# Optimization experiments

Measured on AMD Instinct MI355X. Metric: run time of the kernel, lower is better.

The kernel has to match this reference:

```python
import jax, jax.numpy as jnp
import numpy as np

B, S, D, H = 32, 512, 512, 8  # note: source requires S == D due to swapped shape tuple in multi_head_attention
DK = D // H  # 64
FF = 200     # hard-coded FFN width in source
LN_EPS = 1e-5


def setup_inputs() -> dict:
    key = jax.random.key(0)
    ks = jax.random.split(key, 20)
    s = 0.02
    return {
        "x": jax.random.normal(ks[0], (B, S, D), dtype=jnp.float32),
        # per-head projections, stacked: torch Linear weight shape is [out, in] = [DK, D]
        "Wq": jax.random.normal(ks[1], (H, DK, D), dtype=jnp.float32) * s,
        "bq": jax.random.normal(ks[2], (H, DK), dtype=jnp.float32) * s,
        "Wk": jax.random.normal(ks[3], (H, DK, D), dtype=jnp.float32) * s,
        "bk": jax.random.normal(ks[4], (H, DK), dtype=jnp.float32) * s,
        "Wv": jax.random.normal(ks[5], (H, DK, D), dtype=jnp.float32) * s,
        "bv": jax.random.normal(ks[6], (H, DK), dtype=jnp.float32) * s,
        "Wo": jax.random.normal(ks[7], (D, D), dtype=jnp.float32) * s,
        "bo": jax.random.normal(ks[8], (D,), dtype=jnp.float32) * s,
        "W1": jax.random.normal(ks[9], (FF, D), dtype=jnp.float32) * s,
        "b1": jax.random.normal(ks[10], (FF,), dtype=jnp.float32) * s,
        "W2": jax.random.normal(ks[11], (FF, FF), dtype=jnp.float32) * s,
        "b2": jax.random.normal(ks[12], (FF,), dtype=jnp.float32) * s,
        "W3": jax.random.normal(ks[13], (D, FF), dtype=jnp.float32) * s,
        "b3": jax.random.normal(ks[14], (D,), dtype=jnp.float32) * s,
        # single SHARED LayerNorm over last two dims (S, D)
        "gamma": jnp.ones((S, D), dtype=jnp.float32),
        "beta": jnp.zeros((S, D), dtype=jnp.float32),
    }


def _layernorm2d(y, gamma, beta):
    # torch LayerNorm(normalized_shape=(S, D)): normalize over last two axes, biased variance
    m = jnp.mean(y, axis=(-2, -1), keepdims=True)
    v = jnp.mean(jnp.square(y - m), axis=(-2, -1), keepdims=True)
    return (y - m) * jax.lax.rsqrt(v + LN_EPS) * gamma + beta


def reference(x, Wq, bq, Wk, bk, Wv, bv, Wo, bo, W1, b1, W2, b2, W3, b3, gamma, beta):
    # --- multi-head attention (vectorized over the original per-head Python loop) ---
    q = jnp.einsum('bsd,hkd->bhsk', x, Wq) + bq[None, :, None, :]
    k = jnp.einsum('bsd,hkd->bhsk', x, Wk) + bk[None, :, None, :]
    v = jnp.einsum('bsd,hkd->bhsk', x, Wv) + bv[None, :, None, :]
    scores = jnp.einsum('bhsk,bhtk->bhst', q, k) / jnp.sqrt(jnp.float32(DK))
    attn = jax.nn.softmax(scores, axis=-1)
    heads = jnp.einsum('bhst,bhtk->bhsk', attn, v)          # [B,H,S,DK]
    concat = heads.transpose(0, 2, 1, 3).reshape(B, S, D)    # concat heads along feature dim
    y = jnp.einsum('bsd,ed->bse', concat, Wo) + bo + x       # output proj + residual
    # --- post-attention LayerNorm (shared params) ---
    y = _layernorm2d(y, gamma, beta)
    # --- feed-forward: D -> 200 -> 200 -> D, residual, LayerNorm (same shared LN) ---
    f = jax.nn.relu(jnp.einsum('bsd,fd->bsf', y, W1) + b1)
    f = jax.nn.relu(jnp.einsum('bsf,gf->bsg', f, W2) + b2)
    f = jnp.einsum('bsf,df->bsd', f, W3) + b3
    y = _layernorm2d(f + y, gamma, beta)
    # --- final LayerNorm (same shared LN again) ---
    return _layernorm2d(y, gamma, beta)
```

## Files before the change

kernel.cpp:

```cpp
#include <hip/hip_runtime.h>
#include <hip/hip_bf16.h>
#include <stdint.h>

#define B_  32
#define S_  512
#define D_  512
#define H_  8
#define DK_ 64
#define FF_ 200
#define FFP 256
#define M_  (B_*S_)
#define MSD ((size_t)B_*S_*D_)
#define NQKV 1536

typedef __hip_bfloat16 bf16;
typedef __attribute__((ext_vector_type(8))) short short8;
typedef __attribute__((ext_vector_type(4))) float f32x4;
typedef __attribute__((ext_vector_type(4))) unsigned short us4;

__device__ inline float b2f(bf16 v) { return __bfloat162float(v); }
__device__ inline bf16  f2b(float v){ return __float2bfloat16(v); }
__device__ inline unsigned short f2bu(float v) {
  union { bf16 h; unsigned short u; } cv; cv.h = __float2bfloat16(v); return cv.u;
}
__device__ inline float bu2f(unsigned short u) {
  union { unsigned short u; bf16 h; } cv; cv.u = u; return b2f(cv.h);
}
__device__ __forceinline__ void async16(const bf16* g, bf16* l) {
  __builtin_amdgcn_global_load_lds((const __attribute__((address_space(1))) void*)g,
                                   (__attribute__((address_space(3))) void*)l, 16, 0, 0);
}

__global__ void detect_kernel(const unsigned short* __restrict__ xu, int* __restrict__ flag,
                              float* __restrict__ stats) {
  __shared__ int mx[256];
  const int tid = threadIdx.x;
  if (tid < 192) stats[tid] = 0.f;
  int m = 0;
  for (int i = tid * 2; i < 8192; i += 512) {
    int e = (xu[i] >> 7) & 0xFF;
    m = m > e ? m : e;
  }
  mx[tid] = m;
  __syncthreads();
  for (int st = 128; st; st >>= 1) {
    if (tid < st) mx[tid] = mx[tid] > mx[tid + st] ? mx[tid] : mx[tid + st];
    __syncthreads();
  }
  if (tid == 0) *flag = (mx[0] >= 0xC0) ? 1 : 0;
}

__global__ __launch_bounds__(256) void cvt_x8(const void* __restrict__ in, bf16* __restrict__ out,
                                              const int* __restrict__ flag) {
  const bool f32in = (*flag != 0);
  size_t i = ((size_t)blockIdx.x * 256 + threadIdx.x) * 8;
  const size_t stride = (size_t)gridDim.x * 256 * 8;
  for (; i < MSD; i += stride) {
    if (f32in) {
      const float4 a = ((const float4*)in)[i/4];
      const float4 b = ((const float4*)in)[i/4 + 1];
      uint4 o; unsigned short* po = (unsigned short*)&o;
      po[0]=f2bu(a.x); po[1]=f2bu(a.y); po[2]=f2bu(a.z); po[3]=f2bu(a.w);
      po[4]=f2bu(b.x); po[5]=f2bu(b.y); po[6]=f2bu(b.z); po[7]=f2bu(b.w);
      *(uint4*)((unsigned short*)out + i) = o;
    } else {
      *(uint4*)((unsigned short*)out + i) = *(const uint4*)((const unsigned short*)in + i);
    }
  }
}

struct Seg { const void* src; void* dst; int srcRows, srcK, dstK, total; };
struct Segs { Seg s[16]; unsigned int isbf; };

__global__ __launch_bounds__(256) void cvt_all(Segs sg, const int* __restrict__ flag) {
  const bool f32in = (*flag != 0);
  const int seg = blockIdx.x & 15;
  const Seg sd = sg.s[seg];
  const int stride = (gridDim.x >> 4) * 256;
  const bool nopad = (sd.srcK == sd.dstK);
  for (int i = (blockIdx.x >> 4) * 256 + threadIdx.x; i < sd.total; i += stride) {
    int sidx; bool valid;
    if (nopad) { sidx = i; valid = (i < sd.srcRows * sd.srcK); }
    else {
      int r = i / sd.dstK, c = i - r * sd.dstK;
      valid = (r < sd.srcRows) && (c < sd.srcK);
      sidx = r * sd.srcK + c;
    }
    float v = 0.f;
    if (valid) v = f32in ? ((const float*)sd.src)[sidx] : b2f(((const bf16*)sd.src)[sidx]);
    if (sg.isbf & (1u << seg)) ((unsigned short*)sd.dst)[i] = f2bu(v);
    else                       ((float*)sd.dst)[i] = v;
  }
}

template<int MODE, int STATS>
__global__ __launch_bounds__(256) void gemm_mfma(
    const bf16* __restrict__ A, const bf16* __restrict__ W, const float* __restrict__ bias,
    const bf16* __restrict__ R, bf16* __restrict__ C, int M, int N, int K,
    float* __restrict__ stats)
{
  __shared__ __align__(16) char smem[49152];
  bf16*  As  = (bf16*)smem;
  bf16*  Bs  = (bf16*)(smem + 24576);
  float* Lf  = (float*)smem;
  float* red = (float*)(smem + 16896);

  const int tid  = threadIdx.x;
  const int bm   = blockIdx.x * 128;
  const int bn   = blockIdx.y * 128;
  const int w    = tid >> 6;
  const int lane = tid & 63;
  const int qd   = lane >> 4;
  const int ln   = lane & 15;
  const int wr   = (w >> 1) * 64;
  const int wc   = (w & 1) * 64;

  const int r0 = lane >> 2;
  const int ch = (lane & 3) * 8;
  const bf16* Ag0 = A + (size_t)(bm + w*16 + r0) * K + ch;
  const bf16* Ag1 = Ag0 + (size_t)64 * K;
  const bf16* Bg0 = W + (size_t)(bn + w*16 + r0) * K + ch;
  const bf16* Bg1 = Bg0 + (size_t)64 * K;
  const int lo = w*512 + lane*8;

  f32x4 acc[4][4] = {};
  const int nt = K >> 5;

  async16(Ag0, As + lo);
  async16(Ag1, As + lo + 2048);
  async16(Bg0, Bs + lo);
  async16(Bg1, Bs + lo + 2048);
  async16(Ag0 + 32, As + 4096 + lo);
  async16(Ag1 + 32, As + 4096 + lo + 2048);
  async16(Bg0 + 32, Bs + 4096 + lo);
  async16(Bg1 + 32, Bs + 4096 + lo + 2048);

  int pcur = 0;
  for (int t = 0; t < nt; t++) {
    if (t + 1 < nt) {
      asm volatile("s_waitcnt vmcnt(4)" ::: "memory");
    } else {
      asm volatile("s_waitcnt vmcnt(0)" ::: "memory");
    }
    __builtin_amdgcn_s_barrier();

    const int cur = pcur << 12;
    short8 af[4], bfr[4];
#pragma unroll
    for (int i = 0; i < 4; i++) af[i]  = *(const short8*)(As + cur + (wr + i*16 + ln)*32 + qd*8);
#pragma unroll
    for (int j = 0; j < 4; j++) bfr[j] = *(const short8*)(Bs + cur + (wc + j*16 + ln)*32 + qd*8);

    if (t + 2 < nt) {
      int pst = pcur - 1; if (pst < 0) pst = 2;
      const int nxt = pst << 12;
      const int k0  = (t + 2) << 5;
      async16(Ag0 + k0, As + nxt + lo);
      async16(Ag1 + k0, As + nxt + lo + 2048);
      async16(Bg0 + k0, Bs + nxt + lo);
      async16(Bg1 + k0, Bs + nxt + lo + 2048);
    }

#pragma unroll
    for (int i = 0; i < 4; i++)
#pragma unroll
      for (int j = 0; j < 4; j++)
        acc[i][j] = __builtin_amdgcn_mfma_f32_16x16x32_bf16(af[i], bfr[j], acc[i][j], 0, 0, 0);

    pcur = pcur + 1 == 3 ? 0 : pcur + 1;
  }
  __syncthreads();

  float s_acc = 0.f, ss_acc = 0.f;
  const int lrbase = (w >> 1)*16 + qd*4;
#pragma unroll
  for (int i = 0; i < 4; i++) {
#pragma unroll
    for (int j = 0; j < 4; j++) {
      const int col = wc + j*16 + ln;
#pragma unroll
      for (int rg = 0; rg < 4; rg++)
        Lf[(lrbase + rg)*132 + col] = acc[i][j][rg];
    }
    __syncthreads();
#pragma unroll
    for (int pz = 0; pz < 2; pz++) {
      const int q   = tid + pz*256;
      const int r   = q >> 4;
      const int nof = (q & 15)*8;
      const int m   = bm + (r >> 4)*64 + i*16 + (r & 15);
      const int n   = bn + nof;
      f32x4 v0 = *(const f32x4*)(Lf + r*132 + nof);
      f32x4 v1 = *(const f32x4*)(Lf + r*132 + nof + 4);
      f32x4 b0 = *(const f32x4*)(bias + n);
      f32x4 b1 = *(const f32x4*)(bias + n + 4);
      float vals[8];
#pragma unroll
      for (int e = 0; e < 4; e++) { vals[e] = v0[e] + b0[e]; vals[4+e] = v1[e] + b1[e]; }
      if (MODE == 1) {
#pragma unroll
        for (int e = 0; e < 8; e++) vals[e] = fmaxf(vals[e], 0.f);
      }
      if (MODE == 2) {
        const uint4 rv = *(const uint4*)((const unsigned short*)R + (size_t)m * N + n);
        const unsigned short* rp = (const unsigned short*)&rv;
#pragma unroll
        for (int e = 0; e < 8; e++) vals[e] += bu2f(rp[e]);
      }
      if (STATS) {
#pragma unroll
        for (int e = 0; e < 8; e++) { s_acc += vals[e]; ss_acc += vals[e]*vals[e]; }
      }
      uint4 o; unsigned short* op = (unsigned short*)&o;
#pragma unroll
      for (int e = 0; e < 8; e++) op[e] = f2bu(vals[e]);
      *(uint4*)((unsigned short*)C + (size_t)m * N + n) = o;
    }
    __syncthreads();
  }

  if (STATS) {
    red[tid] = s_acc; red[256 + tid] = ss_acc;
    __syncthreads();
    for (int st = 128; st; st >>= 1) {
      if (tid < st) { red[tid] += red[tid + st]; red[256 + tid] += red[256 + tid + st]; }
      __syncthreads();
    }
    if (tid == 0) {
      const int b = bm >> 9;
      atomicAdd(&stats[b*2],     red[0]);
      atomicAdd(&stats[b*2 + 1], red[256]);
    }
  }
}

__global__ __launch_bounds__(1024, 4) void attn_lds(const bf16* __restrict__ qkv,
                                                    bf16* __restrict__ cat)
{
  __shared__ bf16 Ks[2 * 512 * 32];
  __shared__ bf16 Vs[64 * 520];
  __shared__ bf16 pbuf[16][16][40];

  const int tid  = threadIdx.x;
  const int w    = tid >> 6;
  const int lane = tid & 63;
  const int qd   = lane >> 4;
  const int ln   = lane & 15;
  const int bh   = blockIdx.x;
  const int b    = bh >> 3, h = bh & 7;
  const bf16* base = qkv + (size_t)b * 512 * NQKV + h * 64;

  for (int c = tid; c < 4096; c += 1024) {
    int part = c & 3, key = (c >> 2) & 511, ks = c >> 11;
    async16(base + (size_t)key * NQKV + 512 + ks*32 + part*8, Ks + c*8);
  }
  for (int c = tid; c < 4096; c += 1024) {
    int dkg = c >> 9, key = c & 511;
    uint4 vv = *(const uint4*)(base + (size_t)key * NQKV + 1024 + dkg*8);
    const unsigned short* pv = (const unsigned short*)&vv;
#pragma unroll
    for (int j = 0; j < 8; j++)
      *(unsigned short*)&Vs[(dkg*8 + j)*520 + key] = pv[j];
  }
  short8 bq[2][2];
#pragma unroll
  for (int qt = 0; qt < 2; qt++)
#pragma unroll
    for (int ks = 0; ks < 2; ks++)
      bq[qt][ks] = *(const short8*)(base + (size_t)(w*32 + qt*16 + ln) * NQKV + ks*32 + qd*8);

  __syncthreads();

  bf16 (*pb)[40] = pbuf[w];
  f32x4 o[2][4] = {};
  float l[2] = {0.f, 0.f};

  for (int st = 0; st < 16; st++) {
    short8 ak[2][2];
#pragma unroll
    for (int kt = 0; kt < 2; kt++)
#pragma unroll
      for (int ks = 0; ks < 2; ks++)
        ak[kt][ks] = *(const short8*)(Ks + ks*16384 + (st*32 + kt*16 + ln)*32 + qd*8);
    f32x4 s[2][2] = {};
#pragma unroll
    for (int kt = 0; kt < 2; kt++)
#pragma unroll
      for (int qt = 0; qt < 2; qt++) {
        s[kt][qt] = __builtin_amdgcn_mfma_f32_16x16x32_bf16(ak[kt][0], bq[qt][0], s[kt][qt], 0, 0, 0);
        s[kt][qt] = __builtin_amdgcn_mfma_f32_16x16x32_bf16(ak[kt][1], bq[qt][1], s[kt][qt], 0, 0, 0);
      }
    float e[2][2][4];
#pragma unroll
    for (int kt = 0; kt < 2; kt++)
#pragma unroll
      for (int qt = 0; qt < 2; qt++)
#pragma unroll
        for (int rg = 0; rg < 4; rg++) {
          float ev = __expf(s[kt][qt][rg] * 0.125f);
          e[kt][qt][rg] = ev;
          l[qt] += ev;
        }
#pragma unroll
    for (int qt = 0; qt < 2; qt++) {
#pragma unroll
      for (int kt = 0; kt < 2; kt++) {
        uint2 pk;
        pk.x = (unsigned)f2bu(e[kt][qt][0]) | ((unsigned)f2bu(e[kt][qt][1]) << 16);
        pk.y = (unsigned)f2bu(e[kt][qt][2]) | ((unsigned)f2bu(e[kt][qt][3]) << 16);
        *(uint2*)&pb[ln][kt*16 + qd*4] = pk;
      }
      short8 ap = *(const short8*)&pb[ln][qd*8];
#pragma unroll
      for (int nt = 0; nt < 4; nt++) {
        short8 bv = *(const short8*)(Vs + (nt*16 + ln)*520 + st*32 + qd*8);
        o[qt][nt] = __builtin_amdgcn_mfma_f32_16x16x32_bf16(ap, bv, o[qt][nt], 0, 0, 0);
      }
    }
  }

#pragma unroll
  for (int qt = 0; qt < 2; qt++) {
    l[qt] += __shfl_xor(l[qt], 16);
    l[qt] += __shfl_xor(l[qt], 32);
  }
  float inv0 = 1.f / l[0], inv1 = 1.f / l[1];

  const size_t crow0 = (size_t)(b*S_ + w*32) * D_ + h*DK_;
#pragma unroll
  for (int qt = 0; qt < 2; qt++) {
#pragma unroll
    for (int rg = 0; rg < 4; rg++) {
      float ivv = __shfl(qt ? inv1 : inv0, qd*4 + rg);
      int r = qt*16 + qd*4 + rg;
      bf16* cp = cat + crow0 + (size_t)r * D_ + ln;
#pragma unroll
      for (int nt = 0; nt < 4; nt++) cp[nt*16] = f2b(o[qt][nt][rg] * ivv);
    }
  }
}

__global__ __launch_bounds__(256) void ln_b16_b16(const bf16* __restrict__ in,
    const float* __restrict__ stats, const bf16* __restrict__ gamma,
    const bf16* __restrict__ beta, bf16* __restrict__ out)
{
  const int b = blockIdx.x >> 4;
  const float invN = 1.f / (float)(S_*D_);
  const float m    = stats[b*2] * invN;
  const float var  = stats[b*2+1] * invN - m*m;
  const float rstd = rsqrtf(var + 1e-5f);
  size_t v = (size_t)b * 65536 + (blockIdx.x & 15) * 4096 + threadIdx.x;
#pragma unroll 4
  for (int it = 0; it < 16; it++, v += 256) {
    us4 xi = *(const us4*)((const unsigned short*)in + v*4);
    size_t e = (v * 4) & (S_*D_ - 1);
    us4 g4 = *(const us4*)((const unsigned short*)gamma + e);
    us4 b4 = *(const us4*)((const unsigned short*)beta + e);
    us4 o;
    o[0] = f2bu((bu2f(xi[0]) - m) * rstd * bu2f(g4[0]) + bu2f(b4[0]));
    o[1] = f2bu((bu2f(xi[1]) - m) * rstd * bu2f(g4[1]) + bu2f(b4[1]));
    o[2] = f2bu((bu2f(xi[2]) - m) * rstd * bu2f(g4[2]) + bu2f(b4[2]));
    o[3] = f2bu((bu2f(xi[3]) - m) * rstd * bu2f(g4[3]) + bu2f(b4[3]));
    *(us4*)((unsigned short*)out + v*4) = o;
  }
}

__global__ __launch_bounds__(256) void ln_b16_b16_stats(const bf16* __restrict__ in,
    const float* __restrict__ stats, const bf16* __restrict__ gamma,
    const bf16* __restrict__ beta, bf16* __restrict__ out, float* __restrict__ stats3)
{
  __shared__ float red[512];
  const int b = blockIdx.x >> 4;
  const float invN = 1.f / (float)(S_*D_);
  const float m    = stats[b*2] * invN;
  const float var  = stats[b*2+1] * invN - m*m;
  const float rstd = rsqrtf(var + 1e-5f);
  size_t v = (size_t)b * 65536 + (blockIdx.x & 15) * 4096 + threadIdx.x;
  float s_acc = 0.f, ss_acc = 0.f;
#pragma unroll 4
  for (int it = 0; it < 16; it++, v += 256) {
    us4 xi = *(const us4*)((const unsigned short*)in + v*4);
    size_t e = (v * 4) & (S_*D_ - 1);
    us4 g4 = *(const us4*)((const unsigned short*)gamma + e);
    us4 b4 = *(const us4*)((const unsigned short*)beta + e);
    float o0 = (bu2f(xi[0]) - m) * rstd * bu2f(g4[0]) + bu2f(b4[0]);
    float o1 = (bu2f(xi[1]) - m) * rstd * bu2f(g4[1]) + bu2f(b4[1]);
    float o2 = (bu2f(xi[2]) - m) * rstd * bu2f(g4[2]) + bu2f(b4[2]);
    float o3 = (bu2f(xi[3]) - m) * rstd * bu2f(g4[3]) + bu2f(b4[3]);
    us4 o;
    o[0] = f2bu(o0); o[1] = f2bu(o1); o[2] = f2bu(o2); o[3] = f2bu(o3);
    s_acc  += o0 + o1 + o2 + o3;
    ss_acc += o0*o0 + o1*o1 + o2*o2 + o3*o3;
    *(us4*)((unsigned short*)out + v*4) = o;
  }
  const int tid = threadIdx.x;
  red[tid] = s_acc; red[256 + tid] = ss_acc;
  __syncthreads();
  for (int st = 128; st; st >>= 1) {
    if (tid < st) { red[tid] += red[tid + st]; red[256 + tid] += red[256 + tid + st]; }
    __syncthreads();
  }
  if (tid == 0) {
    atomicAdd(&stats3[b*2],     red[0]);
    atomicAdd(&stats3[b*2 + 1], red[256]);
  }
}

__global__ __launch_bounds__(256) void ln_apply_out(const bf16* __restrict__ in,
    const float* __restrict__ stats, const bf16* __restrict__ gamma,
    const bf16* __restrict__ beta, void* __restrict__ out, const int* __restrict__ flag)
{
  const bool f32 = (*flag != 0);
  const int b = blockIdx.x >> 4;
  const float invN = 1.f / (float)(S_*D_);
  const float m    = stats[b*2] * invN;
  const float var  = stats[b*2+1] * invN - m*m;
  const float rstd = rsqrtf(var + 1e-5f);
  size_t v = (size_t)b * 65536 + (blockIdx.x & 15) * 4096 + threadIdx.x;
#pragma unroll 4
  for (int it = 0; it < 16; it++, v += 256) {
    us4 xi = *(const us4*)((const unsigned short*)in + v*4);
    size_t e = (v * 4) & (S_*D_ - 1);
    us4 g4 = *(const us4*)((const unsigned short*)gamma + e);
    us4 b4 = *(const us4*)((const unsigned short*)beta + e);
    float4 o;
    o.x = (bu2f(xi[0]) - m) * rstd * bu2f(g4[0]) + bu2f(b4[0]);
    o.y = (bu2f(xi[1]) - m) * rstd * bu2f(g4[1]) + bu2f(b4[1]);
    o.z = (bu2f(xi[2]) - m) * rstd * bu2f(g4[2]) + bu2f(b4[2]);
    o.w = (bu2f(xi[3]) - m) * rstd * bu2f(g4[3]) + bu2f(b4[3]);
    if (f32) ((float4*)out)[v] = o;
    else {
      us4 ob;
      ob[0] = f2bu(o.x); ob[1] = f2bu(o.y); ob[2] = f2bu(o.z); ob[3] = f2bu(o.w);
      *(us4*)((unsigned short*)out + v*4) = ob;
    }
  }
}

extern "C" void kernel_launch(void* const* d_in, const int* in_sizes, int n_in,
                              void* d_out, int out_size, void* d_ws, size_t ws_size,
                              hipStream_t stream)
{
  char* p = (char*)d_ws;
  auto alloc_b = [&](size_t elems) { void* r = p; p += elems * 2; return (bf16*)r; };
  auto alloc_f = [&](size_t elems) {
    p = (char*)(((uintptr_t)p + 15) & ~(uintptr_t)15); void* r = p; p += elems * 4; return (float*)r;
  };

  bf16* xb   = alloc_b(MSD);
  bf16* qkv  = alloc_b(3 * MSD);
  bf16* catb = alloc_b(MSD);
  bf16* wqkv = alloc_b(3 * 512 * 512);
  bf16* wo   = alloc_b(512 * 512);
  bf16* w1p  = alloc_b((size_t)FFP * 512);
  bf16* w2p  = alloc_b((size_t)FFP * FFP);
  bf16* w3p  = alloc_b((size_t)512 * FFP);
  bf16* gm   = alloc_b((size_t)S_ * D_);
  bf16* bt   = alloc_b((size_t)S_ * D_);
  float* bqkv= alloc_f(3 * 512);
  float* bo  = alloc_f(512);
  float* b1p = alloc_f(FFP);
  float* b2p = alloc_f(FFP);
  float* b3  = alloc_f(512);
  float* stats = alloc_f(192);
  int*   flag  = (int*)alloc_f(16);
  if ((size_t)(p - (char*)d_ws) > ws_size) return;

  bf16* y1b = qkv;
  bf16* f1  = qkv + MSD;
  bf16* f2  = qkv + MSD + (size_t)M_ * FFP;
  bf16* yA  = qkv + 2 * MSD;
  bf16* yB  = catb;
  bf16* y2b = yA;
  float* st1 = stats, *st2 = stats + 64, *st3 = stats + 128;

  detect_kernel<<<1, 256, 0, stream>>>((const unsigned short*)d_in[0], flag, stats);
  cvt_x8<<<2048, 256, 0, stream>>>(d_in[0], xb, flag);

  Segs sg;
  sg.s[0]  = { d_in[1],  wqkv,               512, 512, 512, 512*512 };
  sg.s[1]  = { d_in[3],  wqkv + 512*512,     512, 512, 512, 512*512 };
  sg.s[2]  = { d_in[5],  wqkv + 2*512*512,   512, 512, 512, 512*512 };
  sg.s[3]  = { d_in[7],  wo,                 512, 512, 512, 512*512 };
  sg.s[4]  = { d_in[9],  w1p,                FF_, 512, 512, FFP*512 };
  sg.s[5]  = { d_in[11], w2p,                FF_, FF_, FFP, FFP*FFP };
  sg.s[6]  = { d_in[13], w3p,                512, FF_, FFP, 512*FFP };
  sg.s[7]  = { d_in[2],  bqkv,               1, 512, 512, 512 };
  sg.s[8]  = { d_in[4],  bqkv + 512,         1, 512, 512, 512 };
  sg.s[9]  = { d_in[6],  bqkv + 1024,        1, 512, 512, 512 };
  sg.s[10] = { d_in[8],  bo,                 1, 512, 512, 512 };
  sg.s[11] = { d_in[10], b1p,                1, FF_, FFP, FFP };
  sg.s[12] = { d_in[12], b2p,                1, FF_, FFP, FFP };
  sg.s[13] = { d_in[14], b3,                 1, 512, 512, 512 };
  sg.s[14] = { d_in[15], gm,                 1, S_*D_, S_*D_, S_*D_ };
  sg.s[15] = { d_in[16], bt,                 1, S_*D_, S_*D_, S_*D_ };
  sg.isbf = 0xC07F;
  cvt_all<<<1024, 256, 0, stream>>>(sg, flag);

  dim3 blk(256);

  gemm_mfma<0, 0><<<dim3(M_/128, NQKV/128), blk, 0, stream>>>(
      xb, wqkv, bqkv, nullptr, qkv, M_, NQKV, 512, nullptr);

  attn_lds<<<B_*H_, 1024, 0, stream>>>(qkv, catb);

  gemm_mfma<2, 1><<<dim3(M_/128, 4), blk, 0, stream>>>(
      catb, wo, bo, xb, yA, M_, 512, 512, st1);

  ln_b16_b16<<<512, blk, 0, stream>>>(yA, st1, gm, bt, y1b);

  gemm_mfma<1, 0><<<dim3(M_/128, 2), blk, 0, stream>>>(
      y1b, w1p, b1p, nullptr, f1, M_, FFP, 512, nullptr);
  gemm_mfma<1, 0><<<dim3(M_/128, 2), blk, 0, stream>>>(
      f1, w2p, b2p, nullptr, f2, M_, FFP, FFP, nullptr);
  gemm_mfma<2, 1><<<dim3(M_/128, 4), blk, 0, stream>>>(
      f2, w3p, b3, y1b, yB, M_, 512, FFP, st2);

  ln_b16_b16_stats<<<512, blk, 0, stream>>>(yB, st2, gm, bt, y2b, st3);
  ln_apply_out<<<512, blk, 0, stream>>>(y2b, st3, gm, bt, d_out, flag);
}
```

Measured before the change: 278.0 us.

## Split K/V staging into halves and overlap second-half loads with compute

```diff
diff --git a/kernel.cpp b/kernel.cpp
--- a/kernel.cpp
+++ b/kernel.cpp
@@ -250,12 +250,17 @@
   const int b    = bh >> 3, h = bh & 7;
   const bf16* base = qkv + (size_t)b * 512 * NQKV + h * 64;
 
-  for (int c = tid; c < 4096; c += 1024) {
-    int part = c & 3, key = (c >> 2) & 511, ks = c >> 11;
-    async16(base + (size_t)key * NQKV + 512 + ks*32 + part*8, Ks + c*8);
-  }
-  for (int c = tid; c < 4096; c += 1024) {
-    int dkg = c >> 9, key = c & 511;
+#pragma unroll
+  for (int r = 0; r < 2; r++) {
+    int c = tid + r*1024;
+    int part = c & 3, key = (c >> 2) & 255, ks = c >> 10;
+    async16(base + (size_t)key * NQKV + 512 + ks*32 + part*8,
+            Ks + ks*16384 + key*32 + part*8);
+  }
+#pragma unroll
+  for (int r = 0; r < 2; r++) {
+    int c = tid + r*1024;
+    int dkg = c >> 8, key = c & 255;
     uint4 vv = *(const uint4*)(base + (size_t)key * NQKV + 1024 + dkg*8);
     const unsigned short* pv = (const unsigned short*)&vv;
 #pragma unroll
@@ -270,52 +275,83 @@
       bq[qt][ks] = *(const short8*)(base + (size_t)(w*32 + qt*16 + ln) * NQKV + ks*32 + qd*8);
 
   __syncthreads();
+
+#pragma unroll
+  for (int r = 0; r < 2; r++) {
+    int c = tid + r*1024;
+    int part = c & 3, key = 256 + ((c >> 2) & 255), ks = c >> 10;
+    async16(base + (size_t)key * NQKV + 512 + ks*32 + part*8,
+            Ks + ks*16384 + key*32 + part*8);
+  }
+  uint4 vhold[2]; int vdst[2];
+#pragma unroll
+  for (int r = 0; r < 2; r++) {
+    int c = tid + r*1024;
+    int dkg = c >> 8, key = 256 + (c & 255);
+    vhold[r] = *(const uint4*)(base + (size_t)key * NQKV + 1024 + dkg*8);
+    vdst[r] = dkg*8*520 + key;
+  }
+  asm volatile("" ::: "memory");
 
   bf16 (*pb)[40] = pbuf[w];
   f32x4 o[2][4] = {};
   float l[2] = {0.f, 0.f};
 
-  for (int st = 0; st < 16; st++) {
-    short8 ak[2][2];
-#pragma unroll
-    for (int kt = 0; kt < 2; kt++)
-#pragma unroll
-      for (int ks = 0; ks < 2; ks++)
-        ak[kt][ks] = *(const short8*)(Ks + ks*16384 + (st*32 + kt*16 + ln)*32 + qd*8);
-    f32x4 s[2][2] = {};
-#pragma unroll
-    for (int kt = 0; kt < 2; kt++)
+  for (int half = 0; half < 2; half++) {
+    for (int st = half*8; st < half*8 + 8; st++) {
+      short8 ak[2][2];
+#pragma unroll
+      for (int kt = 0; kt < 2; kt++)
+#pragma unroll
+        for (int ks = 0; ks < 2; ks++)
+          ak[kt][ks] = *(const short8*)(Ks + ks*16384 + (st*32 + kt*16 + ln)*32 + qd*8);
+      f32x4 s[2][2] = {};
+#pragma unroll
+      for (int kt = 0; kt < 2; kt++)
+#pragma unroll
+        for (int qt = 0; qt < 2; qt++) {
+          s[kt][qt] = __builtin_amdgcn_mfma_f32_16x16x32_bf16(ak[kt][0], bq[qt][0], s[kt][qt], 0, 0, 0);
+          s[kt][qt] = __builtin_amdgcn_mfma_f32_16x16x32_bf16(ak[kt][1], bq[qt][1], s[kt][qt], 0, 0, 0);
+        }
+      float e[2][2][4];
+#pragma unroll
+      for (int kt = 0; kt < 2; kt++)
+#pragma unroll
+        for (int qt = 0; qt < 2; qt++)
+#pragma unroll
+          for (int rg = 0; rg < 4; rg++) {
+            float ev = __expf(s[kt][qt][rg] * 0.125f);
+            e[kt][qt][rg] = ev;
+            l[qt] += ev;
+          }
 #pragma unroll
       for (int qt = 0; qt < 2; qt++) {
-        s[kt][qt] = __builtin_amdgcn_mfma_f32_16x16x32_bf16(ak[kt][0], bq[qt][0], s[kt][qt], 0, 0, 0);
-        s[kt][qt] = __builtin_amdgcn_mfma_f32_16x16x32_bf16(ak[kt][1], bq[qt][1], s[kt][qt], 0, 0, 0);
+#pragma unroll
+        for (int kt = 0; kt < 2; kt++) {
+          uint2 pk;
+          pk.x = (unsigned)f2bu(e[kt][qt][0]) | ((unsigned)f2bu(e[kt][qt][1]) << 16);
+          pk.y = (unsigned)f2bu(e[kt][qt][2]) | ((unsigned)f2bu(e[kt][qt][3]) << 16);
+          *(uint2*)&pb[ln][kt*16 + qd*4] = pk;
+        }
+        short8 ap = *(const short8*)&pb[ln][qd*8];
+#pragma unroll
+        for (int nt = 0; nt < 4; nt++) {
+          short8 bv = *(const short8*)(Vs + (nt*16 + ln)*520 + st*32 + qd*8);
+          o[qt][nt] = __builtin_amdgcn_mfma_f32_16x16x32_bf16(ap, bv, o[qt][nt], 0, 0, 0);
+        }
       }
-    float e[2][2][4];
-#pragma unroll
-    for (int kt = 0; kt < 2; kt++)
-#pragma unroll
-      for (int qt = 0; qt < 2; qt++)
-#pragma unroll
-        for (int rg = 0; rg < 4; rg++) {
-          float ev = __expf(s[kt][qt][rg] * 0.125f);
-          e[kt][qt][rg] = ev;
-          l[qt] += ev;
-        }
-#pragma unroll
-    for (int qt = 0; qt < 2; qt++) {
-#pragma unroll
-      for (int kt = 0; kt < 2; kt++) {
-        uint2 pk;
-        pk.x = (unsigned)f2bu(e[kt][qt][0]) | ((unsigned)f2bu(e[kt][qt][1]) << 16);
-        pk.y = (unsigned)f2bu(e[kt][qt][2]) | ((unsigned)f2bu(e[kt][qt][3]) << 16);
-        *(uint2*)&pb[ln][kt*16 + qd*4] = pk;
+    }
+    if (half == 0) {
+      asm volatile("s_waitcnt vmcnt(0)" ::: "memory");
+#pragma unroll
+      for (int r = 0; r < 2; r++) {
+        const unsigned short* pv = (const unsigned short*)&vhold[r];
+#pragma unroll
+        for (int j = 0; j < 8; j++)
+          *(unsigned short*)&Vs[vdst[r] + j*520] = pv[j];
       }
-      short8 ap = *(const short8*)&pb[ln][qd*8];
-#pragma unroll
-      for (int nt = 0; nt < 4; nt++) {
-        short8 bv = *(const short8*)(Vs + (nt*16 + ln)*520 + st*32 + qd*8);
-        o[qt][nt] = __builtin_amdgcn_mfma_f32_16x16x32_bf16(ap, bv, o[qt][nt], 0, 0, 0);
-      }
+      asm volatile("s_waitcnt lgkmcnt(0)" ::: "memory");
+      __builtin_amdgcn_s_barrier();
     }
   }
 
```

Measured after the change: 276.4 us, median of 2. No clear change (-0.6%).

## Pipeline K/V loads in 128-key chunks overlapping attention compute

Applied to the files above, without the earlier changes.

```diff
diff --git a/kernel.cpp b/kernel.cpp
--- a/kernel.cpp
+++ b/kernel.cpp
@@ -250,17 +250,20 @@
   const int b    = bh >> 3, h = bh & 7;
   const bf16* base = qkv + (size_t)b * 512 * NQKV + h * 64;
 
-  for (int c = tid; c < 4096; c += 1024) {
-    int part = c & 3, key = (c >> 2) & 511, ks = c >> 11;
-    async16(base + (size_t)key * NQKV + 512 + ks*32 + part*8, Ks + c*8);
-  }
-  for (int c = tid; c < 4096; c += 1024) {
-    int dkg = c >> 9, key = c & 511;
-    uint4 vv = *(const uint4*)(base + (size_t)key * NQKV + 1024 + dkg*8);
+  const int kpart = tid & 3;
+  const int kkey  = (tid >> 2) & 127;
+  const int kks   = tid >> 9;
+  const int vdkg  = tid >> 7;
+  const int vkey0 = tid & 127;
+
+  async16(base + (size_t)kkey * NQKV + 512 + kks*32 + kpart*8,
+          Ks + kks*16384 + kkey*32 + kpart*8);
+  {
+    uint4 vv = *(const uint4*)(base + (size_t)vkey0 * NQKV + 1024 + vdkg*8);
     const unsigned short* pv = (const unsigned short*)&vv;
 #pragma unroll
     for (int j = 0; j < 8; j++)
-      *(unsigned short*)&Vs[(dkg*8 + j)*520 + key] = pv[j];
+      *(unsigned short*)&Vs[(vdkg*8 + j)*520 + vkey0] = pv[j];
   }
   short8 bq[2][2];
 #pragma unroll
@@ -270,52 +273,77 @@
       bq[qt][ks] = *(const short8*)(base + (size_t)(w*32 + qt*16 + ln) * NQKV + ks*32 + qd*8);
 
   __syncthreads();
+
+  uint4 vhold[3];
+#pragma unroll
+  for (int c = 1; c < 4; c++) {
+    const int key = c*128 + kkey;
+    async16(base + (size_t)key * NQKV + 512 + kks*32 + kpart*8,
+            Ks + kks*16384 + key*32 + kpart*8);
+    vhold[c-1] = *(const uint4*)(base + (size_t)(c*128 + vkey0) * NQKV + 1024 + vdkg*8);
+  }
+  asm volatile("" ::: "memory");
 
   bf16 (*pb)[40] = pbuf[w];
   f32x4 o[2][4] = {};
   float l[2] = {0.f, 0.f};
 
-  for (int st = 0; st < 16; st++) {
-    short8 ak[2][2];
-#pragma unroll
-    for (int kt = 0; kt < 2; kt++)
-#pragma unroll
-      for (int ks = 0; ks < 2; ks++)
-        ak[kt][ks] = *(const short8*)(Ks + ks*16384 + (st*32 + kt*16 + ln)*32 + qd*8);
-    f32x4 s[2][2] = {};
-#pragma unroll
-    for (int kt = 0; kt < 2; kt++)
+#pragma unroll
+  for (int c = 0; c < 4; c++) {
+    for (int st = c*4; st < c*4 + 4; st++) {
+      short8 ak[2][2];
+#pragma unroll
+      for (int kt = 0; kt < 2; kt++)
+#pragma unroll
+        for (int ks = 0; ks < 2; ks++)
+          ak[kt][ks] = *(const short8*)(Ks + ks*16384 + (st*32 + kt*16 + ln)*32 + qd*8);
+      f32x4 s[2][2] = {};
+#pragma unroll
+      for (int kt = 0; kt < 2; kt++)
+#pragma unroll
+        for (int qt = 0; qt < 2; qt++) {
+          s[kt][qt] = __builtin_amdgcn_mfma_f32_16x16x32_bf16(ak[kt][0], bq[qt][0], s[kt][qt], 0, 0, 0);
+          s[kt][qt] = __builtin_amdgcn_mfma_f32_16x16x32_bf16(ak[kt][1], bq[qt][1], s[kt][qt], 0, 0, 0);
+        }
+      float e[2][2][4];
+#pragma unroll
+      for (int kt = 0; kt < 2; kt++)
+#pragma unroll
+        for (int qt = 0; qt < 2; qt++)
+#pragma unroll
+          for (int rg = 0; rg < 4; rg++) {
+            float ev = __expf(s[kt][qt][rg] * 0.125f);
+            e[kt][qt][rg] = ev;
+            l[qt] += ev;
+          }
 #pragma unroll
       for (int qt = 0; qt < 2; qt++) {
-        s[kt][qt] = __builtin_amdgcn_mfma_f32_16x16x32_bf16(ak[kt][0], bq[qt][0], s[kt][qt], 0, 0, 0);
-        s[kt][qt] = __builtin_amdgcn_mfma_f32_16x16x32_bf16(ak[kt][1], bq[qt][1], s[kt][qt], 0, 0, 0);
+#pragma unroll
+        for (int kt = 0; kt < 2; kt++) {
+          uint2 pk;
+          pk.x = (unsigned)f2bu(e[kt][qt][0]) | ((unsigned)f2bu(e[kt][qt][1]) << 16);
+          pk.y = (unsigned)f2bu(e[kt][qt][2]) | ((unsigned)f2bu(e[kt][qt][3]) << 16);
+          *(uint2*)&pb[ln][kt*16 + qd*4] = pk;
+        }
+        short8 ap = *(const short8*)&pb[ln][qd*8];
+#pragma unroll
+        for (int nt = 0; nt < 4; nt++) {
+          short8 bv = *(const short8*)(Vs + (nt*16 + ln)*520 + st*32 + qd*8);
+          o[qt][nt] = __builtin_amdgcn_mfma_f32_16x16x32_bf16(ap, bv, o[qt][nt], 0, 0, 0);
+        }
       }
-    float e[2][2][4];
-#pragma unroll
-    for (int kt = 0; kt < 2; kt++)
-#pragma unroll
-      for (int qt = 0; qt < 2; qt++)
-#pragma unroll
-        for (int rg = 0; rg < 4; rg++) {
-          float ev = __expf(s[kt][qt][rg] * 0.125f);
-          e[kt][qt][rg] = ev;
-          l[qt] += ev;
-        }
-#pragma unroll
-    for (int qt = 0; qt < 2; qt++) {
-#pragma unroll
-      for (int kt = 0; kt < 2; kt++) {
-        uint2 pk;
-        pk.x = (unsigned)f2bu(e[kt][qt][0]) | ((unsigned)f2bu(e[kt][qt][1]) << 16);
-        pk.y = (unsigned)f2bu(e[kt][qt][2]) | ((unsigned)f2bu(e[kt][qt][3]) << 16);
-        *(uint2*)&pb[ln][kt*16 + qd*4] = pk;
-      }
-      short8 ap = *(const short8*)&pb[ln][qd*8];
-#pragma unroll
-      for (int nt = 0; nt < 4; nt++) {
-        short8 bv = *(const short8*)(Vs + (nt*16 + ln)*520 + st*32 + qd*8);
-        o[qt][nt] = __builtin_amdgcn_mfma_f32_16x16x32_bf16(ap, bv, o[qt][nt], 0, 0, 0);
-      }
+    }
+    if (c < 3) {
+      if (c == 0)      asm volatile("s_waitcnt vmcnt(4)" ::: "memory");
+      else if (c == 1) asm volatile("s_waitcnt vmcnt(2)" ::: "memory");
+      else             asm volatile("s_waitcnt vmcnt(0)" ::: "memory");
+      const unsigned short* pv = (const unsigned short*)&vhold[c];
+      const int vkey = (c+1)*128 + vkey0;
+#pragma unroll
+      for (int j = 0; j < 8; j++)
+        *(unsigned short*)&Vs[(vdkg*8 + j)*520 + vkey] = pv[j];
+      asm volatile("s_waitcnt lgkmcnt(0)" ::: "memory");
+      __builtin_amdgcn_s_barrier();
     }
   }
 
```

Result: slower. 411.0 us (+47.8%).
